# Optimization experiments

Hardware: AMD Instinct MI355X
Metric: run time of the kernel (lower is better)

## Reference

```python
import jax, jax.numpy as jnp
import numpy as np

N_HEADS = 4
D_K = 64
SCALE = D_K ** -0.5


def setup_inputs() -> dict:
    key = jax.random.key(0)
    ks = jax.random.split(key, 5)
    B, C, H, W = 16, 256, 32, 32
    x = jax.random.normal(ks[0], (B, C, H, W), dtype=jnp.float32)
    # projection: Linear(C, 3*h*d_k); stored as [in, out] so y = x @ W + b
    w_proj = jax.random.normal(ks[1], (C, 3 * N_HEADS * D_K), dtype=jnp.float32) * (C ** -0.5)
    b_proj = jax.random.normal(ks[2], (3 * N_HEADS * D_K,), dtype=jnp.float32) * 0.02
    w_out = jax.random.normal(ks[3], (N_HEADS * D_K, C), dtype=jnp.float32) * ((N_HEADS * D_K) ** -0.5)
    b_out = jax.random.normal(ks[4], (C,), dtype=jnp.float32) * 0.02
    return {"x": x, "w_proj": w_proj, "b_proj": b_proj, "w_out": w_out, "b_out": b_out}


def reference(x, w_proj, b_proj, w_out, b_out):
    b, c, h, w = x.shape
    s = h * w
    # [b, c, h, w] -> [b, s, c]  (matches view + permute in torch)
    xf = jnp.transpose(x.reshape(b, c, s), (0, 2, 1))
    # QKV projection -> [b, s, heads, 3*d_k]
    qkv = (xf @ w_proj + b_proj).reshape(b, s, N_HEADS, 3 * D_K)
    q, k, v = jnp.split(qkv, 3, axis=-1)  # each [b, s, heads, d_k]
    # scores [b, i, j, heads]; softmax over j (axis=2), as in the original
    attn = jnp.einsum('bihd,bjhd->bijh', q, k) * SCALE
    attn = jax.nn.softmax(attn, axis=2)
    res = jnp.einsum('bijh,bjhd->bihd', attn, v).reshape(b, s, N_HEADS * D_K)
    res = res @ w_out + b_out + xf  # residual added to un-normalized xf (norm is unused in source)
    return jnp.transpose(res, (0, 2, 1)).reshape(b, c, h, w)
```

## Files before the change

kernel.cpp:

```cpp
#include <hip/hip_runtime.h>
#include <hip/hip_bf16.h>
#include <stdint.h>

typedef float f32x4 __attribute__((ext_vector_type(4)));
typedef float f32x16 __attribute__((ext_vector_type(16)));
typedef __bf16 bf16x8 __attribute__((ext_vector_type(8)));
typedef unsigned short u16x8 __attribute__((ext_vector_type(8)));
typedef int i32x4 __attribute__((ext_vector_type(4)));

#define MFMA16(a, b, c) __builtin_amdgcn_mfma_f32_16x16x32_bf16(a, b, c, 0, 0, 0)
#define MFMA32(a, b, c) __builtin_amdgcn_mfma_f32_32x32x16_bf16(a, b, c, 0, 0, 0)

#define QSCALE 0.18033688011112042f

static __device__ __forceinline__ unsigned short f2bf(float f) {
    uint32_t u = __builtin_bit_cast(uint32_t, f);
    u = u + 0x7FFFu + ((u >> 16) & 1u);
    return (unsigned short)(u >> 16);
}

static __device__ __forceinline__ bf16x8 ldb8(const unsigned short* p) {
    return __builtin_bit_cast(bf16x8, *reinterpret_cast<const u16x8*>(p));
}

static __device__ __forceinline__ void gload16(const void* g, void* l) {
    __builtin_amdgcn_global_load_lds(
        (const __attribute__((address_space(1))) void*)g,
        (__attribute__((address_space(3))) void*)l,
        16, 0, 0);
}

__global__ __launch_bounds__(256) void k_tall(const float* __restrict__ x,
                                              const float* __restrict__ wp,
                                              const float* __restrict__ wo,
                                              unsigned short* __restrict__ xT,
                                              unsigned short* __restrict__ wpT,
                                              unsigned short* __restrict__ woT) {
    int bid = blockIdx.x;
    const float* src; unsigned short* dst; int Cc, nCT; int lb;
    if (bid < 1024)      { src = x;  dst = xT;  Cc = 1024; nCT = 16; lb = bid; }
    else if (bid < 1072) { src = wp; dst = wpT; Cc = 768;  nCT = 12; lb = bid - 1024; }
    else                 { src = wo; dst = woT; Cc = 256;  nCT = 4;  lb = bid - 1072; }
    int R = 256, nRT = 4;
    int ct = lb % nCT;
    int rt = (lb / nCT) % nRT;
    int b  = lb / (nCT * nRT);
    int t = threadIdx.x;
    __shared__ __align__(16) unsigned short tile[64][72];
    int tr = t >> 2, tc = (t & 3) * 16;
    const float* sp = src + ((size_t)(b * R + rt * 64 + tr)) * Cc + ct * 64 + tc;
#pragma unroll
    for (int j = 0; j < 4; ++j) {
        float4 v = reinterpret_cast<const float4*>(sp)[j];
        ushort4 hv; hv.x = f2bf(v.x); hv.y = f2bf(v.y); hv.z = f2bf(v.z); hv.w = f2bf(v.w);
        *reinterpret_cast<ushort4*>(&tile[tr][tc + 4 * j]) = hv;
    }
    __syncthreads();
    int c = t >> 2, rs = (t & 3) * 16;
    u16x8 o0, o1;
#pragma unroll
    for (int z = 0; z < 8; ++z) o0[z] = tile[rs + z][c];
#pragma unroll
    for (int z = 0; z < 8; ++z) o1[z] = tile[rs + 8 + z][c];
    unsigned short* dp = dst + ((size_t)b * Cc + ct * 64 + c) * R + rt * 64 + rs;
    *reinterpret_cast<u16x8*>(dp) = o0;
    *reinterpret_cast<u16x8*>(dp + 8) = o1;
}

__global__ __launch_bounds__(256) void k_gemm_qkv(const unsigned short* __restrict__ xT,
                                                  const unsigned short* __restrict__ wT,
                                                  const float* __restrict__ bias,
                                                  unsigned short* __restrict__ qkv,
                                                  unsigned short* __restrict__ vT) {
    int bid = blockIdx.x;
    int mt = bid / 6, nt = bid - mt * 6;
    int tid = threadIdx.x;
    int w = tid >> 6, l = tid & 63;
    int l15 = l & 15, lg = l >> 4;
    int wm = (w >> 1) * 64, wn = (w & 1) * 64;

    __shared__ __align__(16) unsigned short Al[128 * 32];
    __shared__ __align__(16) unsigned short Bl[128 * 32];

    f32x4 acc[4][4] = {};

    const char* Agb = (const char*)xT + (size_t)mt * 128 * 512;
    const char* Bgb = (const char*)wT + (size_t)nt * 128 * 512;
    int r0 = w * 32;
    size_t lrow_off = (size_t)(r0 + (l >> 2)) * 512 + (l & 3) * 16;

    for (int kt = 0; kt < 256; kt += 32) {
        __syncthreads();
        const char* ag = Agb + lrow_off + kt * 2;
        const char* bg = Bgb + lrow_off + kt * 2;
        gload16(ag,             (char*)Al + r0 * 64);
        gload16(ag + 16 * 512,  (char*)Al + r0 * 64 + 1024);
        gload16(bg,             (char*)Bl + r0 * 64);
        gload16(bg + 16 * 512,  (char*)Bl + r0 * 64 + 1024);
        __syncthreads();
        bf16x8 af[4], bfr[4];
#pragma unroll
        for (int mi = 0; mi < 4; ++mi)
            af[mi] = ldb8(&Al[(wm + mi * 16 + l15) * 32 + lg * 8]);
#pragma unroll
        for (int ni = 0; ni < 4; ++ni)
            bfr[ni] = ldb8(&Bl[(wn + ni * 16 + l15) * 32 + lg * 8]);
#pragma unroll
        for (int mi = 0; mi < 4; ++mi)
#pragma unroll
            for (int ni = 0; ni < 4; ++ni)
                acc[mi][ni] = MFMA16(af[mi], bfr[ni], acc[mi][ni]);
    }

#pragma unroll
    for (int ni = 0; ni < 4; ++ni) {
        int n0 = nt * 128 + wn + ni * 16;
        int n  = n0 + l15;
        int c0 = n0 % 192;
        float bz = bias[n];
        if (c0 >= 128) {
            int hq = n / 192;
            int d  = (n % 192) - 128;
#pragma unroll
            for (int mi = 0; mi < 4; ++mi) {
                int mg = mt * 128 + wm + mi * 16 + lg * 4;
                int bI = mg >> 10, s = mg & 1023;
                ushort4 hv;
                hv.x = f2bf(acc[mi][ni][0] + bz);
                hv.y = f2bf(acc[mi][ni][1] + bz);
                hv.z = f2bf(acc[mi][ni][2] + bz);
                hv.w = f2bf(acc[mi][ni][3] + bz);
                *reinterpret_cast<ushort4*>(vT + ((size_t)(bI * 4 + hq) * 64 + d) * 1024 + s) = hv;
            }
        } else {
            float qs = (c0 < 64) ? QSCALE : 1.0f;
#pragma unroll
            for (int mi = 0; mi < 4; ++mi) {
                int mg = mt * 128 + wm + mi * 16 + lg * 4;
                unsigned short* qp = qkv + (size_t)mg * 768 + n;
#pragma unroll
                for (int r = 0; r < 4; ++r)
                    qp[(size_t)r * 768] = f2bf((acc[mi][ni][r] + bz) * qs);
            }
        }
    }
}

#define PACKJK(SV, R, OUT) do { \
    int pa_, pb_, pc_, pd_; \
    asm("v_cvt_pk_bf16_f32 %0, %1, %2" : "=v"(pa_) : "v"(SV[R + 0]), "v"(SV[R + 1])); \
    asm("v_cvt_pk_bf16_f32 %0, %1, %2" : "=v"(pb_) : "v"(SV[R + 2]), "v"(SV[R + 3])); \
    asm("v_cvt_pk_bf16_f32 %0, %1, %2" : "=v"(pc_) : "v"(SV[R + 4]), "v"(SV[R + 5])); \
    asm("v_cvt_pk_bf16_f32 %0, %1, %2" : "=v"(pd_) : "v"(SV[R + 6]), "v"(SV[R + 7])); \
    int pu_ = hi ? pa_ : pc_;  int psu_ = __shfl_xor(pu_, 32); \
    int pv_ = hi ? pb_ : pd_;  int psv_ = __shfl_xor(pv_, 32); \
    i32x4 pri_ = { hi ? psu_ : pa_, hi ? psv_ : pb_, hi ? pc_ : psu_, hi ? pd_ : psv_ }; \
    OUT = __builtin_bit_cast(bf16x8, pri_); \
} while (0)

__global__ __launch_bounds__(128) void k_attn(const unsigned short* __restrict__ qkv,
                                              const unsigned short* __restrict__ vT,
                                              unsigned short* __restrict__ ao) {
    int bid = blockIdx.x;
    int qt = bid & 15;
    int h  = (bid >> 4) & 3;
    int b  = bid >> 6;
    int tid = threadIdx.x;
    int w = tid >> 6;
    int l = tid & 63;
    int l31 = l & 31;
    int hi = l >> 5;
    int x7 = l & 7;

    __shared__ __align__(16) unsigned short Kl[64 * 64];
    __shared__ __align__(16) unsigned short Vl[64 * 64];

    const size_t bb = (size_t)b * 1024;
    const int bh = b * 4 + h;

    bf16x8 qf[4];
    int qg0 = qt * 64 + w * 32 + l31;
#pragma unroll
    for (int dk = 0; dk < 4; ++dk)
        qf[dk] = ldb8(qkv + (bb + qg0) * 768 + h * 192 + dk * 16 + hi * 8);

    int colB[4];
#pragma unroll
    for (int c = 0; c < 4; ++c) colB[c] = ((2 * c + hi) ^ x7) * 8;

    int srow = w * 32 + (l >> 3);
    int gsw  = (l & 7) ^ (srow & 7);
    const unsigned short* ksrc = qkv + (bb + srow) * 768 + h * 192 + 64 + gsw * 8;
    const unsigned short* vsrc = vT + ((size_t)bh * 64 + srow) * 1024 + gsw * 8;

    float mrow = -1e30f, lrow = 0.0f;
    f32x16 oacc0 = {}, oacc1 = {};

    for (int jt = 0; jt < 1024; jt += 64) {
        __syncthreads();
#pragma unroll
        for (int i = 0; i < 4; ++i) {
            gload16(ksrc + (size_t)i * 8 * 768, (char*)Kl + (w * 32 + i * 8) * 128);
            gload16(vsrc + (size_t)i * 8 * 1024, (char*)Vl + (w * 32 + i * 8) * 128);
        }
        __syncthreads();

        f32x16 st0 = {}, st1 = {};
#pragma unroll
        for (int dk = 0; dk < 4; ++dk) {
            bf16x8 k0 = ldb8(&Kl[(l31) * 64 + colB[dk]]);
            bf16x8 k1 = ldb8(&Kl[(32 + l31) * 64 + colB[dk]]);
            st0 = MFMA32(k0, qf[dk], st0);
            st1 = MFMA32(k1, qf[dk], st1);
        }

        float pm = st0[0];
#pragma unroll
        for (int r = 1; r < 16; ++r) pm = fmaxf(pm, st0[r]);
#pragma unroll
        for (int r = 0; r < 16; ++r) pm = fmaxf(pm, st1[r]);
        pm = fmaxf(pm, __shfl_xor(pm, 32));

        if (!__all(pm - mrow <= 8.0f)) {
            float mn = fmaxf(mrow, pm);
            float ef = __builtin_amdgcn_exp2f(mrow - mn);
            mrow = mn;
            lrow *= ef;
#pragma unroll
            for (int r = 0; r < 16; ++r) {
                int qr = (r & 3) + 8 * (r >> 2) + hi * 4;
                float efq = __shfl(ef, qr);
                oacc0[r] *= efq;
                oacc1[r] *= efq;
            }
        }

        float rs = 0.0f;
#pragma unroll
        for (int r = 0; r < 16; ++r) { st0[r] = __builtin_amdgcn_exp2f(st0[r] - mrow); rs += st0[r]; }
#pragma unroll
        for (int r = 0; r < 16; ++r) { st1[r] = __builtin_amdgcn_exp2f(st1[r] - mrow); rs += st1[r]; }
        rs += __shfl_xor(rs, 32);
        lrow += rs;

        bf16x8 pf0, pf1, pf2, pf3;
        PACKJK(st0, 0, pf0);
        PACKJK(st0, 8, pf1);
        PACKJK(st1, 0, pf2);
        PACKJK(st1, 8, pf3);

#pragma unroll
        for (int jk = 0; jk < 4; ++jk) {
            bf16x8 pfk = (jk == 0) ? pf0 : (jk == 1) ? pf1 : (jk == 2) ? pf2 : pf3;
            bf16x8 v0 = ldb8(&Vl[(l31) * 64 + colB[jk]]);
            bf16x8 v1 = ldb8(&Vl[(32 + l31) * 64 + colB[jk]]);
            oacc0 = MFMA32(pfk, v0, oacc0);
            oacc1 = MFMA32(pfk, v1, oacc1);
        }

        ksrc += (size_t)64 * 768;
        vsrc += 64;
    }

    float rcp = 1.0f / lrow;
#pragma unroll
    for (int r = 0; r < 16; ++r) {
        int qr = (r & 3) + 8 * (r >> 2) + hi * 4;
        float lq = __shfl(rcp, qr);
        int qg = qt * 64 + w * 32 + qr;
        size_t o = (bb + qg) * 256 + h * 64 + l31;
        ao[o]      = f2bf(oacc0[r] * lq);
        ao[o + 32] = f2bf(oacc1[r] * lq);
    }
}

__global__ __launch_bounds__(256) void k_gemm_out(const unsigned short* __restrict__ aoin,
                                                  const unsigned short* __restrict__ wT,
                                                  const float* __restrict__ bias,
                                                  const float* __restrict__ x,
                                                  float* __restrict__ out) {
    int bid = blockIdx.x;
    int mt = bid >> 1, nt = bid & 1;
    int tid = threadIdx.x;
    int w = tid >> 6, l = tid & 63;
    int l15 = l & 15, lg = l >> 4;
    int wm = (w >> 1) * 64, wn = (w & 1) * 64;

    __shared__ __align__(16) unsigned short Al[128 * 32];
    __shared__ __align__(16) unsigned short Bl[128 * 32];

    f32x4 acc[4][4] = {};

    const char* Agb = (const char*)aoin + (size_t)mt * 128 * 512;
    const char* Bgb = (const char*)wT + (size_t)nt * 128 * 512;
    int r0 = w * 32;
    size_t lrow_off = (size_t)(r0 + (l >> 2)) * 512 + (l & 3) * 16;

    for (int kt = 0; kt < 256; kt += 32) {
        __syncthreads();
        const char* ag = Agb + lrow_off + kt * 2;
        const char* bg = Bgb + lrow_off + kt * 2;
        gload16(ag,             (char*)Al + r0 * 64);
        gload16(ag + 16 * 512,  (char*)Al + r0 * 64 + 1024);
        gload16(bg,             (char*)Bl + r0 * 64);
        gload16(bg + 16 * 512,  (char*)Bl + r0 * 64 + 1024);
        __syncthreads();
        bf16x8 af[4], bfr[4];
#pragma unroll
        for (int mi = 0; mi < 4; ++mi)
            af[mi] = ldb8(&Al[(wm + mi * 16 + l15) * 32 + lg * 8]);
#pragma unroll
        for (int ni = 0; ni < 4; ++ni)
            bfr[ni] = ldb8(&Bl[(wn + ni * 16 + l15) * 32 + lg * 8]);
#pragma unroll
        for (int mi = 0; mi < 4; ++mi)
#pragma unroll
            for (int ni = 0; ni < 4; ++ni)
                acc[mi][ni] = MFMA16(af[mi], bfr[ni], acc[mi][ni]);
    }

#pragma unroll
    for (int ni = 0; ni < 4; ++ni) {
        int n = nt * 128 + wn + ni * 16 + l15;
        float bz = bias[n];
#pragma unroll
        for (int mi = 0; mi < 4; ++mi) {
            int mg = mt * 128 + wm + mi * 16 + lg * 4;
            int bI = mg >> 10, i = mg & 1023;
            size_t o = (((size_t)(bI * 256 + n)) << 10) + i;
            float4 xr = *reinterpret_cast<const float4*>(x + o);
            float4 res;
            res.x = acc[mi][ni][0] + bz + xr.x;
            res.y = acc[mi][ni][1] + bz + xr.y;
            res.z = acc[mi][ni][2] + bz + xr.z;
            res.w = acc[mi][ni][3] + bz + xr.w;
            *reinterpret_cast<float4*>(out + o) = res;
        }
    }
}

extern "C" void kernel_launch(void* const* d_in, const int* in_sizes, int n_in,
                              void* d_out, int out_size, void* d_ws, size_t ws_size,
                              hipStream_t stream) {
    const float* x      = (const float*)d_in[0];
    const float* w_proj = (const float*)d_in[1];
    const float* b_proj = (const float*)d_in[2];
    const float* w_out  = (const float*)d_in[3];
    const float* b_out  = (const float*)d_in[4];
    float* out = (float*)d_out;

    char* ws = (char*)d_ws;
    unsigned short* xT     = (unsigned short*)(ws);
    unsigned short* wprojT = (unsigned short*)(ws + 8388608);
    unsigned short* woutT  = (unsigned short*)(ws + 8781824);
    unsigned short* qkv    = (unsigned short*)(ws + 8912896);
    unsigned short* ao     = (unsigned short*)(ws + 34078720);
    unsigned short* vT     = (unsigned short*)(ws + 42467328);

    k_tall<<<1088, 256, 0, stream>>>(x, w_proj, w_out, xT, wprojT, woutT);
    k_gemm_qkv<<<768, 256, 0, stream>>>(xT, wprojT, b_proj, qkv, vT);
    k_attn<<<1024, 128, 0, stream>>>(qkv, vT, ao);
    k_gemm_out<<<256, 256, 0, stream>>>(ao, woutT, b_out, x, out);
}
```

Baseline: 137.2 us.

## Process two query tiles per attention block to reuse K/V tiles

Each attention block now handles 128 query rows (two independent 64-row groups per wave pair) instead of 64, so every K/V tile loaded into shared memory is used twice. The grid is halved from 1024 to 512 blocks. This cuts global-to-LDS traffic and barrier overhead per query, but doubles the accumulator and Q registers per thread, which may lower occupancy. On a GPU with 256 CUs, 512 blocks also gives fewer waves to hide latency.

```diff
diff --git a/kernel.cpp b/kernel.cpp
--- a/kernel.cpp
+++ b/kernel.cpp
@@ -158,13 +158,63 @@
     OUT = __builtin_bit_cast(bf16x8, pri_); \
 } while (0)
 
+#define PROCESS(QF, MROW, LROW, OA, OB) do {                                              \
+    f32x16 st0 = {}, st1 = {};                                                            \
+    _Pragma("unroll")                                                                     \
+    for (int dk = 0; dk < 4; ++dk) {                                                      \
+        bf16x8 k0 = ldb8(&Kl[(l31) * 64 + colB[dk]]);                                     \
+        bf16x8 k1 = ldb8(&Kl[(32 + l31) * 64 + colB[dk]]);                                \
+        st0 = MFMA32(k0, QF[dk], st0);                                                    \
+        st1 = MFMA32(k1, QF[dk], st1);                                                    \
+    }                                                                                     \
+    float pm = st0[0];                                                                    \
+    _Pragma("unroll")                                                                     \
+    for (int r = 1; r < 16; ++r) pm = fmaxf(pm, st0[r]);                                  \
+    _Pragma("unroll")                                                                     \
+    for (int r = 0; r < 16; ++r) pm = fmaxf(pm, st1[r]);                                  \
+    pm = fmaxf(pm, __shfl_xor(pm, 32));                                                   \
+    if (!__all(pm - MROW <= 8.0f)) {                                                      \
+        float mn = fmaxf(MROW, pm);                                                       \
+        float ef = __builtin_amdgcn_exp2f(MROW - mn);                                     \
+        MROW = mn;                                                                        \
+        LROW *= ef;                                                                       \
+        _Pragma("unroll")                                                                 \
+        for (int r = 0; r < 16; ++r) {                                                    \
+            int qr = (r & 3) + 8 * (r >> 2) + hi * 4;                                     \
+            float efq = __shfl(ef, qr);                                                   \
+            OA[r] *= efq;                                                                 \
+            OB[r] *= efq;                                                                 \
+        }                                                                                 \
+    }                                                                                     \
+    float rs = 0.0f;                                                                      \
+    _Pragma("unroll")                                                                     \
+    for (int r = 0; r < 16; ++r) { st0[r] = __builtin_amdgcn_exp2f(st0[r] - MROW); rs += st0[r]; } \
+    _Pragma("unroll")                                                                     \
+    for (int r = 0; r < 16; ++r) { st1[r] = __builtin_amdgcn_exp2f(st1[r] - MROW); rs += st1[r]; } \
+    rs += __shfl_xor(rs, 32);                                                             \
+    LROW += rs;                                                                           \
+    bf16x8 pf0, pf1, pf2, pf3;                                                            \
+    PACKJK(st0, 0, pf0);                                                                  \
+    PACKJK(st0, 8, pf1);                                                                  \
+    PACKJK(st1, 0, pf2);                                                                  \
+    PACKJK(st1, 8, pf3);                                                                  \
+    _Pragma("unroll")                                                                     \
+    for (int jk = 0; jk < 4; ++jk) {                                                      \
+        bf16x8 pfk = (jk == 0) ? pf0 : (jk == 1) ? pf1 : (jk == 2) ? pf2 : pf3;           \
+        bf16x8 v0 = ldb8(&Vl[(l31) * 64 + colB[jk]]);                                     \
+        bf16x8 v1 = ldb8(&Vl[(32 + l31) * 64 + colB[jk]]);                                \
+        OA = MFMA32(pfk, v0, OA);                                                         \
+        OB = MFMA32(pfk, v1, OB);                                                         \
+    }                                                                                     \
+} while (0)
+
 __global__ __launch_bounds__(128) void k_attn(const unsigned short* __restrict__ qkv,
                                               const unsigned short* __restrict__ vT,
                                               unsigned short* __restrict__ ao) {
     int bid = blockIdx.x;
-    int qt = bid & 15;
-    int h  = (bid >> 4) & 3;
-    int b  = bid >> 6;
+    int qt = bid & 7;
+    int h  = (bid >> 3) & 3;
+    int b  = bid >> 5;
     int tid = threadIdx.x;
     int w = tid >> 6;
     int l = tid & 63;
@@ -178,11 +228,13 @@
     const size_t bb = (size_t)b * 1024;
     const int bh = b * 4 + h;
 
-    bf16x8 qf[4];
-    int qg0 = qt * 64 + w * 32 + l31;
-#pragma unroll
-    for (int dk = 0; dk < 4; ++dk)
-        qf[dk] = ldb8(qkv + (bb + qg0) * 768 + h * 192 + dk * 16 + hi * 8);
+    bf16x8 qfA[4], qfB[4];
+    int qgA = qt * 128 + w * 32 + l31;
+#pragma unroll
+    for (int dk = 0; dk < 4; ++dk) {
+        qfA[dk] = ldb8(qkv + (bb + qgA) * 768 + h * 192 + dk * 16 + hi * 8);
+        qfB[dk] = ldb8(qkv + (bb + qgA + 64) * 768 + h * 192 + dk * 16 + hi * 8);
+    }
 
     int colB[4];
 #pragma unroll
@@ -193,8 +245,8 @@
     const unsigned short* ksrc = qkv + (bb + srow) * 768 + h * 192 + 64 + gsw * 8;
     const unsigned short* vsrc = vT + ((size_t)bh * 64 + srow) * 1024 + gsw * 8;
 
-    float mrow = -1e30f, lrow = 0.0f;
-    f32x16 oacc0 = {}, oacc1 = {};
+    float mrowA = -1e30f, lrowA = 0.0f, mrowB = -1e30f, lrowB = 0.0f;
+    f32x16 oA0 = {}, oA1 = {}, oB0 = {}, oB1 = {};
 
     for (int jt = 0; jt < 1024; jt += 64) {
         __syncthreads();
@@ -205,72 +257,27 @@
         }
         __syncthreads();
 
-        f32x16 st0 = {}, st1 = {};
-#pragma unroll
-        for (int dk = 0; dk < 4; ++dk) {
-            bf16x8 k0 = ldb8(&Kl[(l31) * 64 + colB[dk]]);
-            bf16x8 k1 = ldb8(&Kl[(32 + l31) * 64 + colB[dk]]);
-            st0 = MFMA32(k0, qf[dk], st0);
-            st1 = MFMA32(k1, qf[dk], st1);
-        }
-
-        float pm = st0[0];
-#pragma unroll
-        for (int r = 1; r < 16; ++r) pm = fmaxf(pm, st0[r]);
-#pragma unroll
-        for (int r = 0; r < 16; ++r) pm = fmaxf(pm, st1[r]);
-        pm = fmaxf(pm, __shfl_xor(pm, 32));
-
-        if (!__all(pm - mrow <= 8.0f)) {
-            float mn = fmaxf(mrow, pm);
-            float ef = __builtin_amdgcn_exp2f(mrow - mn);
-            mrow = mn;
-            lrow *= ef;
-#pragma unroll
-            for (int r = 0; r < 16; ++r) {
-                int qr = (r & 3) + 8 * (r >> 2) + hi * 4;
-                float efq = __shfl(ef, qr);
-                oacc0[r] *= efq;
-                oacc1[r] *= efq;
-            }
-        }
-
-        float rs = 0.0f;
-#pragma unroll
-        for (int r = 0; r < 16; ++r) { st0[r] = __builtin_amdgcn_exp2f(st0[r] - mrow); rs += st0[r]; }
-#pragma unroll
-        for (int r = 0; r < 16; ++r) { st1[r] = __builtin_amdgcn_exp2f(st1[r] - mrow); rs += st1[r]; }
-        rs += __shfl_xor(rs, 32);
-        lrow += rs;
-
-        bf16x8 pf0, pf1, pf2, pf3;
-        PACKJK(st0, 0, pf0);
-        PACKJK(st0, 8, pf1);
-        PACKJK(st1, 0, pf2);
-        PACKJK(st1, 8, pf3);
-
-#pragma unroll
-        for (int jk = 0; jk < 4; ++jk) {
-            bf16x8 pfk = (jk == 0) ? pf0 : (jk == 1) ? pf1 : (jk == 2) ? pf2 : pf3;
-            bf16x8 v0 = ldb8(&Vl[(l31) * 64 + colB[jk]]);
-            bf16x8 v1 = ldb8(&Vl[(32 + l31) * 64 + colB[jk]]);
-            oacc0 = MFMA32(pfk, v0, oacc0);
-            oacc1 = MFMA32(pfk, v1, oacc1);
-        }
+        PROCESS(qfA, mrowA, lrowA, oA0, oA1);
+        PROCESS(qfB, mrowB, lrowB, oB0, oB1);
 
         ksrc += (size_t)64 * 768;
         vsrc += 64;
     }
 
-    float rcp = 1.0f / lrow;
+    float rcpA = 1.0f / lrowA;
+    float rcpB = 1.0f / lrowB;
 #pragma unroll
     for (int r = 0; r < 16; ++r) {
         int qr = (r & 3) + 8 * (r >> 2) + hi * 4;
-        float lq = __shfl(rcp, qr);
-        int qg = qt * 64 + w * 32 + qr;
-        size_t o = (bb + qg) * 256 + h * 64 + l31;
-        ao[o]      = f2bf(oacc0[r] * lq);
-        ao[o + 32] = f2bf(oacc1[r] * lq);
+        float lqA = __shfl(rcpA, qr);
+        float lqB = __shfl(rcpB, qr);
+        int qg = qt * 128 + w * 32 + qr;
+        size_t oA = (bb + qg) * 256 + h * 64 + l31;
+        size_t oB = (bb + qg + 64) * 256 + h * 64 + l31;
+        ao[oA]      = f2bf(oA0[r] * lqA);
+        ao[oA + 32] = f2bf(oA1[r] * lqA);
+        ao[oB]      = f2bf(oB0[r] * lqB);
+        ao[oB + 32] = f2bf(oB1[r] * lqB);
     }
 }
 
@@ -359,6 +366,6 @@
 
     k_tall<<<1088, 256, 0, stream>>>(x, w_proj, w_out, xT, wprojT, woutT);
     k_gemm_qkv<<<768, 256, 0, stream>>>(xT, wprojT, b_proj, qkv, vT);
-    k_attn<<<1024, 128, 0, stream>>>(qkv, vT, ao);
+    k_attn<<<512, 128, 0, stream>>>(qkv, vT, ao);
     k_gemm_out<<<256, 256, 0, stream>>>(ao, woutT, b_out, x, out);
 }
```

Result: slower. 145.3 us (+5.9%).

## Load K/V fragments directly from global memory and reorder block mapping by query tile

Applied to the files above, without the earlier changes.

The attention kernel no longer stages K and V tiles in LDS with two barriers per iteration. Each lane now reads its MFMA operand fragments straight from global memory. Block indices are also remapped so consecutive blocks cover different batch-head pairs for the same query tile. The goal is to remove barrier and LDS round-trip overhead and rely on L2/L1 for reuse across the two waves and across blocks. The risks are duplicated global loads from both waves, with less coalesced 16-byte accesses, and exposed load latency because there is no explicit prefetch.

```diff
diff --git a/kernel.cpp b/kernel.cpp
--- a/kernel.cpp
+++ b/kernel.cpp
@@ -162,21 +162,17 @@
                                               const unsigned short* __restrict__ vT,
                                               unsigned short* __restrict__ ao) {
     int bid = blockIdx.x;
-    int qt = bid & 15;
-    int h  = (bid >> 4) & 3;
-    int b  = bid >> 6;
+    int qt = bid >> 6;
+    int bh = bid & 63;
+    int b  = bh >> 2;
+    int h  = bh & 3;
     int tid = threadIdx.x;
     int w = tid >> 6;
     int l = tid & 63;
     int l31 = l & 31;
     int hi = l >> 5;
-    int x7 = l & 7;
-
-    __shared__ __align__(16) unsigned short Kl[64 * 64];
-    __shared__ __align__(16) unsigned short Vl[64 * 64];
 
     const size_t bb = (size_t)b * 1024;
-    const int bh = b * 4 + h;
 
     bf16x8 qf[4];
     int qg0 = qt * 64 + w * 32 + l31;
@@ -184,32 +180,22 @@
     for (int dk = 0; dk < 4; ++dk)
         qf[dk] = ldb8(qkv + (bb + qg0) * 768 + h * 192 + dk * 16 + hi * 8);
 
-    int colB[4];
-#pragma unroll
-    for (int c = 0; c < 4; ++c) colB[c] = ((2 * c + hi) ^ x7) * 8;
-
-    int srow = w * 32 + (l >> 3);
-    int gsw  = (l & 7) ^ (srow & 7);
-    const unsigned short* ksrc = qkv + (bb + srow) * 768 + h * 192 + 64 + gsw * 8;
-    const unsigned short* vsrc = vT + ((size_t)bh * 64 + srow) * 1024 + gsw * 8;
+    const unsigned short* kR0 = qkv + (bb + l31) * 768 + h * 192 + 64;
+    const unsigned short* kR1 = kR0 + (size_t)32 * 768;
+    const unsigned short* vR0 = vT + ((size_t)bh * 64 + l31) * 1024;
+    const unsigned short* vR1 = vR0 + (size_t)32 * 1024;
 
     float mrow = -1e30f, lrow = 0.0f;
     f32x16 oacc0 = {}, oacc1 = {};
 
     for (int jt = 0; jt < 1024; jt += 64) {
-        __syncthreads();
-#pragma unroll
-        for (int i = 0; i < 4; ++i) {
-            gload16(ksrc + (size_t)i * 8 * 768, (char*)Kl + (w * 32 + i * 8) * 128);
-            gload16(vsrc + (size_t)i * 8 * 1024, (char*)Vl + (w * 32 + i * 8) * 128);
-        }
-        __syncthreads();
-
+        const unsigned short* k0p = kR0 + (size_t)jt * 768;
+        const unsigned short* k1p = kR1 + (size_t)jt * 768;
         f32x16 st0 = {}, st1 = {};
 #pragma unroll
         for (int dk = 0; dk < 4; ++dk) {
-            bf16x8 k0 = ldb8(&Kl[(l31) * 64 + colB[dk]]);
-            bf16x8 k1 = ldb8(&Kl[(32 + l31) * 64 + colB[dk]]);
+            bf16x8 k0 = ldb8(k0p + (2 * dk + hi) * 8);
+            bf16x8 k1 = ldb8(k1p + (2 * dk + hi) * 8);
             st0 = MFMA32(k0, qf[dk], st0);
             st1 = MFMA32(k1, qf[dk], st1);
         }
@@ -249,17 +235,16 @@
         PACKJK(st1, 0, pf2);
         PACKJK(st1, 8, pf3);
 
+        const unsigned short* v0p = vR0 + jt;
+        const unsigned short* v1p = vR1 + jt;
 #pragma unroll
         for (int jk = 0; jk < 4; ++jk) {
             bf16x8 pfk = (jk == 0) ? pf0 : (jk == 1) ? pf1 : (jk == 2) ? pf2 : pf3;
-            bf16x8 v0 = ldb8(&Vl[(l31) * 64 + colB[jk]]);
-            bf16x8 v1 = ldb8(&Vl[(32 + l31) * 64 + colB[jk]]);
+            bf16x8 v0 = ldb8(v0p + (2 * jk + hi) * 8);
+            bf16x8 v1 = ldb8(v1p + (2 * jk + hi) * 8);
             oacc0 = MFMA32(pfk, v0, oacc0);
             oacc1 = MFMA32(pfk, v1, oacc1);
         }
-
-        ksrc += (size_t)64 * 768;
-        vsrc += 64;
     }
 
     float rcp = 1.0f / lrow;
```

Result: slower. 163.4 us (+19.1%).
